# Performance work log

Hardware: AMD Instinct MI355X
Metric: run time of the kernel (lower is better)

## Reference

```python
import jax, jax.numpy as jnp
import numpy as np

ALPHA = 0.2  # LeakyReLU negative slope
N, F_IN, F_OUT = 8192, 512, 64
NEG_BIG = -9e15


def setup_inputs() -> dict:
    key = jax.random.key(0)
    k1, k2, k3, k4 = jax.random.split(key, 4)
    h = jax.random.normal(k1, (N, F_IN), dtype=jnp.float32)
    # xavier_uniform with gain 1.414
    lim_w = 1.414 * np.sqrt(6.0 / (F_IN + F_OUT))
    W = jax.random.uniform(k2, (F_IN, F_OUT), dtype=jnp.float32, minval=-lim_w, maxval=lim_w)
    lim_a = 1.414 * np.sqrt(6.0 / (2 * F_OUT + 1))
    a = jax.random.uniform(k3, (2 * F_OUT, 1), dtype=jnp.float32, minval=-lim_a, maxval=lim_a)
    adj = jax.random.randint(k4, (N, N), 0, 2, dtype=jnp.int32)
    return {"h": h, "W": W, "a": a, "adj": adj}


def reference(h, W, a, adj):
    Wh = h @ W                                  # [N, F_OUT]
    f_out = Wh.shape[1]
    a1 = a[:f_out, 0]                            # source half of attention vector
    a2 = a[f_out:, 0]                            # target half
    # e_ij = LeakyReLU(Wh_i . a1 + Wh_j . a2); equals cat([Wh_i, Wh_j]) @ a
    e = jax.nn.leaky_relu(jnp.matmul(Wh, a1)[:, None] + jnp.matmul(Wh, a2)[None, :], ALPHA)  # [N, N]
    attention = jnp.where(adj > 0, e, NEG_BIG)
    attention = jax.nn.softmax(attention, axis=1)
    # dropout is a no-op at inference (training=False)
    h_prime = attention @ Wh                     # [N, F_OUT]
    return jax.nn.elu(h_prime)                   # concat=True -> ELU
```

## Files before the change

### kernel.cpp

```cpp
#include <hip/hip_runtime.h>
#include <hip/hip_bf16.h>


typedef _Float16 f16;
typedef _Float16 f16x2 __attribute__((ext_vector_type(2)));
typedef _Float16 f16x4 __attribute__((ext_vector_type(4)));
typedef _Float16 f16x8 __attribute__((ext_vector_type(8)));
typedef float f32x4 __attribute__((ext_vector_type(4)));
typedef int   i32x4 __attribute__((ext_vector_type(4)));

#define GAT_N 8192
#define GAT_FIN 512
#define GAT_FOUT 64
#define GAT_ALPHA 0.2f
#define GAT_L2E 1.44269504088896340736f

__global__ void k0_wtrans(const float* __restrict__ W, f16* __restrict__ WT) {
    int idx = blockIdx.x * blockDim.x + threadIdx.x;
    int k = idx >> 6, c = idx & 63;
    WT[c * GAT_FIN + k] = (f16)W[idx];
}

__global__ __launch_bounds__(256) void k1_gemm(const float* __restrict__ h,
        const f16* __restrict__ WT, const float* __restrict__ a,
        f16* __restrict__ WhT, float* __restrict__ s1, float* __restrict__ s2) {
    __shared__ float pacc[4][4][64][4];
    __shared__ float s1red[4][16], s2red[4][16];

    int tid = threadIdx.x;
    int w = tid >> 6, lane = tid & 63;
    int l15 = lane & 15, quad = lane >> 4;
    int rb = blockIdx.x * 16;
    size_t arow = (size_t)(rb + l15) * GAT_FIN;

    f32x4 acc[4] = {};
#pragma unroll
    for (int ks = 0; ks < 4; ks++) {
        int kb = w * 128 + ks * 32 + quad * 8;
        const float4* hp = (const float4*)(h + arow + kb);
        float4 h0 = hp[0], h1 = hp[1];
        f16x8 af = { (f16)h0.x, (f16)h0.y, (f16)h0.z, (f16)h0.w,
                     (f16)h1.x, (f16)h1.y, (f16)h1.z, (f16)h1.w };
#pragma unroll
        for (int t = 0; t < 4; t++) {
            f16x8 bf = *(const f16x8*)(WT + (t * 16 + l15) * GAT_FIN + kb);
            acc[t] = __builtin_amdgcn_mfma_f32_16x16x32_f16(af, bf, acc[t], 0, 0, 0);
        }
    }
#pragma unroll
    for (int t = 0; t < 4; t++)
        *(f32x4*)&pacc[w][t][lane][0] = acc[t];
    __syncthreads();

    float a1v = a[w * 16 + l15];
    float a2v = a[GAT_FOUT + w * 16 + l15];
    float vreg[4];
#pragma unroll
    for (int reg = 0; reg < 4; reg++) {
        float v = 0.f;
#pragma unroll
        for (int ww = 0; ww < 4; ww++) v += pacc[ww][w][lane][reg];
        vreg[reg] = v;
    }
    f16x4 pk = { (f16)vreg[0], (f16)vreg[1], (f16)vreg[2], (f16)vreg[3] };
    *(f16x4*)(WhT + (size_t)(w * 16 + l15) * GAT_N + rb + quad * 4) = pk;

#pragma unroll
    for (int reg = 0; reg < 4; reg++) {
        float c1 = vreg[reg] * a1v, c2 = vreg[reg] * a2v;
#pragma unroll
        for (int off = 1; off < 16; off <<= 1) {
            c1 += __shfl_xor(c1, off);
            c2 += __shfl_xor(c2, off);
        }
        if (l15 == 0) { s1red[w][quad * 4 + reg] = c1; s2red[w][quad * 4 + reg] = c2; }
    }
    __syncthreads();
    if (tid < 16) {
        float t1 = 0.f, t2 = 0.f;
#pragma unroll
        for (int ww = 0; ww < 4; ww++) { t1 += s1red[ww][tid]; t2 += s2red[ww][tid]; }
        s1[rb + tid] = t1;
        s2[rb + tid] = t2;
    }
}

__global__ __launch_bounds__(512, 2) void k3_attn(const int* __restrict__ adj,
        const f16* __restrict__ WhT, const float* __restrict__ s1,
        const float* __restrict__ s2, float* __restrict__ out) {
    __shared__ __align__(16) char smem[2 * 16 * 520 * 2];
    f16* pbuf = (f16*)smem;
    float (*accbuf)[16][64] = (float (*)[16][64])smem;
    __shared__ float dbuf2[16];
    __shared__ float mred[8];

    int tid = threadIdx.x;
    int w = tid >> 6, lane = tid & 63;
    int l15 = lane & 15, quad = lane >> 4;
    int hhalf = lane >> 5, q = lane & 31;
    int rb = blockIdx.x * 16;
    int r = 2 * w + hhalf;

    float m = -1e30f;
    for (int i = tid; i < GAT_N; i += 512) m = fmaxf(m, s2[i]);
#pragma unroll
    for (int off = 32; off >= 1; off >>= 1) m = fmaxf(m, __shfl_xor(m, off));
    if (lane == 0) mred[w] = m;
    __syncthreads();
    float mxv = mred[0];
#pragma unroll
    for (int ww = 1; ww < 8; ww++) mxv = fmaxf(mxv, mred[ww]);

    float s1r = s1[rb + r];
    float cr = s1r + mxv;
    cr = fmaxf(cr, GAT_ALPHA * cr);
    float mcrl = -cr * GAT_L2E;
    const int* adjrow = adj + (size_t)(rb + r) * GAT_N;

    float dacc = 0.f;
    f32x4 acc[4] = {};
    i32x4  avA[4], avB[4];
    float4 svA[4], svB[4];

    auto loadreg = [&](i32x4 (&av_)[4], float4 (&sv_)[4], int rd) {
#pragma unroll
        for (int p = 0; p < 4; p++) {
            int c0 = rd * 512 + p * 128 + q * 4;
            av_[p] = __builtin_nontemporal_load((const i32x4*)(adjrow + c0));
            sv_[p] = *(const float4*)(s2 + c0);
        }
    };

    auto stage = [&](const i32x4 (&av_)[4], const float4 (&sv_)[4], int bb) {
#pragma unroll
        for (int p = 0; p < 4; p++) {
            float svv[4] = { sv_[p].x, sv_[p].y, sv_[p].z, sv_[p].w };
            int base = (4 * p + (q >> 3)) * 520 + ((q >> 1) & 3) * 128 + r * 8 + (q & 1) * 4;
            f16 pf[4];
#pragma unroll
            for (int j = 0; j < 4; j++) {
                float x = s1r + svv[j];
                float e = fmaxf(x, GAT_ALPHA * x);
                float pv = exp2f(fmaf(e, GAT_L2E, mcrl));
                pv = (av_[p][j] > 0) ? pv : 0.0f;
                dacc += pv;
                pf[j] = (f16)pv;
            }
            f16x4 pk = { pf[0], pf[1], pf[2], pf[3] };
            *(f16x4*)&pbuf[bb * 8320 + base] = pk;
        }
    };

    auto round = [&](int rd, int b, const i32x4 (&avP)[4], const float4 (&svP)[4],
                     i32x4 (&avF)[4], float4 (&svF)[4]) {
        f16x8 bfr[2][4];
#pragma unroll
        for (int sl = 0; sl < 2; sl++) {
            int kb = rd * 512 + (2 * w + sl) * 32 + quad * 8;
#pragma unroll
            for (int t = 0; t < 4; t++)
                bfr[sl][t] = *(const f16x8*)(WhT + (size_t)(t * 16 + l15) * GAT_N + kb);
        }
        if (rd < 14) loadreg(avF, svF, rd + 2);
#pragma unroll
        for (int sl = 0; sl < 2; sl++) {
            f16x8 af = *(const f16x8*)&pbuf[b * 8320 + (2 * w + sl) * 520 + lane * 8];
#pragma unroll
            for (int t = 0; t < 4; t++)
                acc[t] = __builtin_amdgcn_mfma_f32_16x16x32_f16(af, bfr[sl][t], acc[t], 0, 0, 0);
        }
        if (rd < 15) stage(avP, svP, 1 - b);
        __syncthreads();
    };

    loadreg(avA, svA, 0);
    stage(avA, svA, 0);
    loadreg(avB, svB, 1);
    __syncthreads();

#pragma unroll 1
    for (int rd = 0; rd < 16; rd += 2) {
        round(rd,     0, avB, svB, avA, svA);
        round(rd + 1, 1, avA, svA, avB, svB);
    }

#pragma unroll
    for (int t = 0; t < 4; t++)
#pragma unroll
        for (int reg = 0; reg < 4; reg++)
            accbuf[w][quad * 4 + reg][t * 16 + l15] = acc[t][reg];
#pragma unroll
    for (int off = 16; off >= 1; off >>= 1) dacc += __shfl_xor(dacc, off);
    if (q == 0) dbuf2[r] = dacc;
    __syncthreads();

    for (int o = tid; o < 16 * 64; o += 512) {
        int rr = o >> 6, c = o & 63;
        float num = 0.f;
#pragma unroll
        for (int ww = 0; ww < 8; ww++) num += accbuf[ww][rr][c];
        float hp = num / dbuf2[rr];
        out[(size_t)(rb + rr) * GAT_FOUT + c] = hp > 0.f ? hp : expm1f(hp);
    }
}

extern "C" void kernel_launch(void* const* d_in, const int* in_sizes, int n_in,
                              void* d_out, int out_size, void* d_ws, size_t ws_size,
                              hipStream_t stream) {
    const float* h   = (const float*)d_in[0];
    const float* W   = (const float*)d_in[1];
    const float* a   = (const float*)d_in[2];
    const int*   adj = (const int*)d_in[3];
    float* out = (float*)d_out;

    char* ws = (char*)d_ws;
    f16*   WT  = (f16*)ws;
    f16*   WhT = (f16*)(ws + 65536);
    float* s1  = (float*)(ws + 65536 + 1048576);
    float* s2  = (float*)(ws + 65536 + 1048576 + 32768);

    k0_wtrans<<<128, 256, 0, stream>>>(W, WT);
    k1_gemm<<<512, 256, 0, stream>>>(h, WT, a, WhT, s1, s2);
    k3_attn<<<512, 512, 0, stream>>>(adj, WhT, s1, s2, out);
}
```

Measured before the change: 427.1 us.

## Cache s2 in LDS, use lgkm-only barriers, restructure attention pipeline

Copies s2 into shared memory during the max reduction so staging reads it from LDS instead of global memory. Replaces __syncthreads with a barrier that waits only on LDS counters, so outstanding non-temporal adj loads can stay in flight across the barrier. WhT operands are now loaded inline next to each MFMA instead of being prefetched into registers before the adj loads. The launch bound is raised to 4 blocks per CU, which tightens the register budget and adds 32KB of LDS per block, risking spills or lower occupancy.

```diff
diff --git a/kernel.cpp b/kernel.cpp
--- a/kernel.cpp
+++ b/kernel.cpp
@@ -15,6 +15,12 @@
 #define GAT_ALPHA 0.2f
 #define GAT_L2E 1.44269504088896340736f
 
+#define BAR_LGKM() do { \
+    asm volatile("s_waitcnt lgkmcnt(0)" ::: "memory"); \
+    __builtin_amdgcn_s_barrier(); \
+    asm volatile("" ::: "memory"); \
+} while (0)
+
 __global__ void k0_wtrans(const float* __restrict__ W, f16* __restrict__ WT) {
     int idx = blockIdx.x * blockDim.x + threadIdx.x;
     int k = idx >> 6, c = idx & 63;
@@ -85,12 +91,13 @@
     }
 }
 
-__global__ __launch_bounds__(512, 2) void k3_attn(const int* __restrict__ adj,
+__global__ __launch_bounds__(512, 4) void k3_attn(const int* __restrict__ adj,
         const f16* __restrict__ WhT, const float* __restrict__ s1,
         const float* __restrict__ s2, float* __restrict__ out) {
     __shared__ __align__(16) char smem[2 * 16 * 520 * 2];
     f16* pbuf = (f16*)smem;
     float (*accbuf)[16][64] = (float (*)[16][64])smem;
+    __shared__ __align__(16) float s2l[GAT_N];
     __shared__ float dbuf2[16];
     __shared__ float mred[8];
 
@@ -102,7 +109,11 @@
     int r = 2 * w + hhalf;
 
     float m = -1e30f;
-    for (int i = tid; i < GAT_N; i += 512) m = fmaxf(m, s2[i]);
+    for (int i = tid; i < GAT_N; i += 512) {
+        float v = s2[i];
+        s2l[i] = v;
+        m = fmaxf(m, v);
+    }
 #pragma unroll
     for (int off = 32; off >= 1; off >>= 1) m = fmaxf(m, __shfl_xor(m, off));
     if (lane == 0) mred[w] = m;
@@ -119,22 +130,21 @@
 
     float dacc = 0.f;
     f32x4 acc[4] = {};
-    i32x4  avA[4], avB[4];
-    float4 svA[4], svB[4];
-
-    auto loadreg = [&](i32x4 (&av_)[4], float4 (&sv_)[4], int rd) {
+    i32x4 avA[4], avB[4];
+
+    auto loadadj = [&](i32x4 (&av_)[4], int rd) {
+#pragma unroll
+        for (int p = 0; p < 4; p++)
+            av_[p] = __builtin_nontemporal_load(
+                (const i32x4*)(adjrow + rd * 512 + p * 128 + q * 4));
+    };
+
+    auto stage = [&](const i32x4 (&av_)[4], int rdS, int bb) {
 #pragma unroll
         for (int p = 0; p < 4; p++) {
-            int c0 = rd * 512 + p * 128 + q * 4;
-            av_[p] = __builtin_nontemporal_load((const i32x4*)(adjrow + c0));
-            sv_[p] = *(const float4*)(s2 + c0);
-        }
-    };
-
-    auto stage = [&](const i32x4 (&av_)[4], const float4 (&sv_)[4], int bb) {
-#pragma unroll
-        for (int p = 0; p < 4; p++) {
-            float svv[4] = { sv_[p].x, sv_[p].y, sv_[p].z, sv_[p].w };
+            int c0 = rdS * 512 + p * 128 + q * 4;
+            float4 sv4 = *(const float4*)&s2l[c0];
+            float svv[4] = { sv4.x, sv4.y, sv4.z, sv4.w };
             int base = (4 * p + (q >> 3)) * 520 + ((q >> 1) & 3) * 128 + r * 8 + (q & 1) * 4;
             f16 pf[4];
 #pragma unroll
@@ -151,37 +161,34 @@
         }
     };
 
-    auto round = [&](int rd, int b, const i32x4 (&avP)[4], const float4 (&svP)[4],
-                     i32x4 (&avF)[4], float4 (&svF)[4]) {
-        f16x8 bfr[2][4];
-#pragma unroll
-        for (int sl = 0; sl < 2; sl++) {
-            int kb = rd * 512 + (2 * w + sl) * 32 + quad * 8;
-#pragma unroll
-            for (int t = 0; t < 4; t++)
-                bfr[sl][t] = *(const f16x8*)(WhT + (size_t)(t * 16 + l15) * GAT_N + kb);
-        }
-        if (rd < 14) loadreg(avF, svF, rd + 2);
+    auto mmaround = [&](int rd, int b) {
 #pragma unroll
         for (int sl = 0; sl < 2; sl++) {
             f16x8 af = *(const f16x8*)&pbuf[b * 8320 + (2 * w + sl) * 520 + lane * 8];
-#pragma unroll
-            for (int t = 0; t < 4; t++)
-                acc[t] = __builtin_amdgcn_mfma_f32_16x16x32_f16(af, bfr[sl][t], acc[t], 0, 0, 0);
-        }
-        if (rd < 15) stage(avP, svP, 1 - b);
-        __syncthreads();
+            int kb = rd * 512 + (2 * w + sl) * 32 + quad * 8;
+#pragma unroll
+            for (int t = 0; t < 4; t++) {
+                f16x8 bf = *(const f16x8*)(WhT + (size_t)(t * 16 + l15) * GAT_N + kb);
+                acc[t] = __builtin_amdgcn_mfma_f32_16x16x32_f16(af, bf, acc[t], 0, 0, 0);
+            }
+        }
     };
 
-    loadreg(avA, svA, 0);
-    stage(avA, svA, 0);
-    loadreg(avB, svB, 1);
-    __syncthreads();
+    loadadj(avA, 0);
+    stage(avA, 0, 0);
+    loadadj(avB, 1);
+    BAR_LGKM();
 
 #pragma unroll 1
     for (int rd = 0; rd < 16; rd += 2) {
-        round(rd,     0, avB, svB, avA, svA);
-        round(rd + 1, 1, avA, svA, avB, svB);
+        mmaround(rd, 0);
+        if (rd + 2 < 16) loadadj(avA, rd + 2);
+        stage(avB, rd + 1, 1);
+        BAR_LGKM();
+        mmaround(rd + 1, 1);
+        if (rd + 3 < 16) loadadj(avB, rd + 3);
+        if (rd + 2 < 16) stage(avA, rd + 2, 0);
+        BAR_LGKM();
     }
 
 #pragma unroll
```

New measurement: 406.1 us. 4.9% less time.
